# Optimization experiments

Measured on AMD Instinct MI355X. Metric: run time of the kernel, lower is better.

## Reference

```python
import jax, jax.numpy as jnp
import numpy as np

T = 2048        # tokens (single causal sequence)
HID = 2048      # hidden_size
H = 16          # num_heads
DN = 128        # qk_nope_head_dim
DR = 64         # qk_rope_head_dim
DQK = DN + DR   # 192
DV = 128        # v_head_dim
QLR = 1536      # q_lora_rank
KVLR = 512      # kv_lora_rank
INTER = 10944   # intermediate_size
EPS = 1e-6
THETA = 10000.0


def rmsnorm(x, w, eps=EPS):
    var = jnp.mean(jnp.square(x), axis=-1, keepdims=True)
    return x * jax.lax.rsqrt(var + eps) * w


def _deinterleave(x):
    # view(b,h,d//2,2).transpose(3,2).reshape(b,h,d): [x0,x2,...,x1,x3,...]
    t, h, d = x.shape
    return x.reshape(t, h, d // 2, 2).swapaxes(-1, -2).reshape(t, h, d)


def _rotate_half(x):
    d = x.shape[-1]
    return jnp.concatenate([-x[..., d // 2:], x[..., :d // 2]], axis=-1)


def setup_inputs() -> dict:
    key = jax.random.key(0)
    ks = jax.random.split(key, 12)
    s = 0.02
    hidden_states = jax.random.normal(ks[0], (T, HID), jnp.float32)
    # real rotary cos/sin tables over the rope slice
    inv_freq = 1.0 / (THETA ** (np.arange(0, DR, 2, dtype=np.float64) / DR))
    freqs = np.outer(np.arange(T, dtype=np.float64), inv_freq)
    emb = np.concatenate([freqs, freqs], axis=-1)  # (T, DR)
    cos = jnp.asarray(np.cos(emb), jnp.float32)[:, None, :]
    sin = jnp.asarray(np.sin(emb), jnp.float32)[:, None, :]
    return {
        "hidden_states": hidden_states,
        "cos": cos,
        "sin": sin,
        "ln_input": jnp.ones((HID,), jnp.float32),
        "w_q_a": jax.random.normal(ks[1], (QLR, HID), jnp.float32) * s,
        "ln_q_a": jnp.ones((QLR,), jnp.float32),
        "w_q_b": jax.random.normal(ks[2], (H * DQK, QLR), jnp.float32) * s,
        "w_kv_a": jax.random.normal(ks[3], (KVLR + DR, HID), jnp.float32) * s,
        "ln_kv_a": jnp.ones((KVLR,), jnp.float32),
        "w_kv_b": jax.random.normal(ks[4], (H * (DN + DV), KVLR), jnp.float32) * s,
        "w_o": jax.random.normal(ks[5], (HID, H * DV), jnp.float32) * s,
        "ln_post": jnp.ones((HID,), jnp.float32),
        "w_gate": jax.random.normal(ks[6], (INTER, HID), jnp.float32) * s,
        "w_up": jax.random.normal(ks[7], (INTER, HID), jnp.float32) * s,
        "w_down": jax.random.normal(ks[8], (HID, INTER), jnp.float32) * s,
    }


def reference(hidden_states, cos, sin, ln_input, w_q_a, ln_q_a, w_q_b,
              w_kv_a, ln_kv_a, w_kv_b, w_o, ln_post, w_gate, w_up, w_down):
    residual = hidden_states
    h = rmsnorm(hidden_states, ln_input)

    # --- MLA attention ---
    # low-rank Q: q_a -> rmsnorm -> q_b
    q = rmsnorm(h @ w_q_a.T, ln_q_a) @ w_q_b.T          # (T, H*DQK)
    q = q.reshape(T, H, DQK)
    q_nope, q_pe = q[..., :DN], q[..., DN:]

    # low-rank KV with shared rope part (MQA-style)
    ckv = h @ w_kv_a.T                                   # (T, KVLR+DR)
    c_kv, k_pe = ckv[:, :KVLR], ckv[:, KVLR:]
    c_kv = rmsnorm(c_kv, ln_kv_a)
    kv = (c_kv @ w_kv_b.T).reshape(T, H, DN + DV)
    k_nope, v = kv[..., :DN], kv[..., DN:]

    # interleaved RoPE on the rope slice
    qp = _deinterleave(q_pe)
    kp = _deinterleave(k_pe.reshape(T, 1, DR))
    q_emb = qp * cos + _rotate_half(qp) * sin            # (T,H,DR)
    k_emb = kp * cos + _rotate_half(kp) * sin            # (T,1,DR)

    q_full = jnp.concatenate([q_nope, q_emb], axis=-1)                          # (T,H,DQK)
    k_full = jnp.concatenate([k_nope, jnp.broadcast_to(k_emb, (T, H, DR))], -1)  # (T,H,DQK)

    scaling = DQK ** -0.5
    scores = jnp.einsum('qhd,khd->hqk', q_full, k_full) * scaling  # (H,T,T)
    idx = jnp.arange(T)
    causal = idx[None, :] <= idx[:, None]                          # (q,k)
    scores = jnp.where(causal[None, :, :], scores, jnp.finfo(scores.dtype).min)
    probs = jax.nn.softmax(scores, axis=-1)
    attn = jnp.einsum('hqk,khd->qhd', probs, v)                    # (T,H,DV)
    attn_out = attn.reshape(T, H * DV) @ w_o.T                     # (T,HID)

    residual = residual + attn_out
    h2 = rmsnorm(residual, ln_post)

    # --- gated MLP (SiLU) ---
    mlp = (jax.nn.silu(h2 @ w_gate.T) * (h2 @ w_up.T)) @ w_down.T
    return residual + mlp
```

## Files before the change

### kernel.cpp

```cpp
#include <hip/hip_runtime.h>
#include <hip/hip_bf16.h>
#include <cstdint>
#include <cstddef>

#define T_SEQ 2048
#define NH 16
#define DQK 192
#define DV 128

typedef __attribute__((ext_vector_type(8))) short short8;
typedef __attribute__((ext_vector_type(4))) float f32x4;

__device__ __forceinline__ void load_lds_16(const void* g, void* l) {
    __builtin_amdgcn_global_load_lds(
        (const __attribute__((address_space(1))) void*)g,
        (__attribute__((address_space(3))) void*)l, 16, 0, 0);
}

__global__ void cvt_pad(const float* __restrict__ in, __hip_bfloat16* __restrict__ out,
                        long n_real, long n_pad) {
    long i = ((long)blockIdx.x * blockDim.x + threadIdx.x) * 4;
    const long stride = (long)gridDim.x * blockDim.x * 4;
    for (; i < n_pad; i += stride) {
        float v0 = 0.f, v1 = 0.f, v2 = 0.f, v3 = 0.f;
        if (i < n_real) {
            const float4 v = *(const float4*)(in + i);
            v0 = v.x; v1 = v.y; v2 = v.z; v3 = v.w;
        }
        out[i + 0] = __float2bfloat16(v0);
        out[i + 1] = __float2bfloat16(v1);
        out[i + 2] = __float2bfloat16(v2);
        out[i + 3] = __float2bfloat16(v3);
    }
}

__global__ __launch_bounds__(256) void rmsnorm_bf16(
    const float* __restrict__ x, const float* __restrict__ w,
    __hip_bfloat16* __restrict__ y, int D, int ldx) {
    const int row = blockIdx.x;
    const float* xr = x + (size_t)row * ldx;
    float ss = 0.f;
    for (int i = threadIdx.x; i < D; i += 256) { float v = xr[i]; ss += v * v; }
    for (int off = 32; off > 0; off >>= 1) ss += __shfl_down(ss, off);
    __shared__ float part[4];
    if ((threadIdx.x & 63) == 0) part[threadIdx.x >> 6] = ss;
    __syncthreads();
    const float tot = part[0] + part[1] + part[2] + part[3];
    const float rs = rsqrtf(tot / (float)D + 1e-6f);
    __hip_bfloat16* yr = y + (size_t)row * D;
    for (int i = threadIdx.x; i < D; i += 256)
        yr[i] = __float2bfloat16(xr[i] * rs * w[i]);
}

template<int EPI>
__global__ __launch_bounds__(256) void gemm_bt(
    const __hip_bfloat16* __restrict__ A, const __hip_bfloat16* __restrict__ B,
    float* __restrict__ Cf, __hip_bfloat16* __restrict__ Cb,
    const float* __restrict__ Add, int N, int K) {
    __shared__ __hip_bfloat16 As[128 * 32];
    __shared__ __hip_bfloat16 Bs[128 * 32];
    const int tid = threadIdx.x;
    const int wave = tid >> 6;
    const int lane = tid & 63;
    const int col = lane & 15;
    const int quad = lane >> 4;
    const long bm = (long)blockIdx.y * 128;
    const long bn = (long)blockIdx.x * 128;
    const int wm = (wave & 1) * 64;
    const int wn = (wave >> 1) * 64;

    const int f0 = tid * 8;
    const int r0 = f0 >> 5, c0 = f0 & 31;
    const int f1 = (256 + tid) * 8;
    const int r1 = f1 >> 5, c1 = f1 & 31;
    __hip_bfloat16* dstA0 = &As[wave * 512];
    __hip_bfloat16* dstA1 = &As[2048 + wave * 512];
    __hip_bfloat16* dstB0 = &Bs[wave * 512];
    __hip_bfloat16* dstB1 = &Bs[2048 + wave * 512];

    f32x4 acc[4][4];
    for (int i = 0; i < 4; i++)
        for (int j = 0; j < 4; j++) acc[i][j] = (f32x4){0.f, 0.f, 0.f, 0.f};

    for (int k0 = 0; k0 < K; k0 += 32) {
        __syncthreads();
        load_lds_16(A + (bm + r0) * (long)K + k0 + c0, dstA0);
        load_lds_16(A + (bm + r1) * (long)K + k0 + c1, dstA1);
        load_lds_16(B + (bn + r0) * (long)K + k0 + c0, dstB0);
        load_lds_16(B + (bn + r1) * (long)K + k0 + c1, dstB1);
        __syncthreads();
        short8 a[4], b[4];
        for (int i = 0; i < 4; i++)
            a[i] = *(const short8*)&As[(wm + 16 * i + col) * 32 + quad * 8];
        for (int j = 0; j < 4; j++)
            b[j] = *(const short8*)&Bs[(wn + 16 * j + col) * 32 + quad * 8];
        for (int i = 0; i < 4; i++)
            for (int j = 0; j < 4; j++)
                acc[i][j] = __builtin_amdgcn_mfma_f32_16x16x32_bf16(a[i], b[j], acc[i][j], 0, 0, 0);
    }

    for (int i = 0; i < 4; i++) {
        const long gm = bm + wm + 16 * i + quad * 4;
        for (int j = 0; j < 4; j++) {
            const long gn = bn + wn + 16 * j + col;
            if (gn < N) {
                for (int r = 0; r < 4; r++) {
                    const long idx = (gm + r) * (long)N + gn;
                    const float a0 = acc[i][j][r];
                    if (EPI == 0) {
                        Cf[idx] = a0;
                    } else if (EPI == 1) {
                        Cf[idx] = a0 + Add[idx];
                    } else if (EPI == 2) {
                        const float s = a0 / (1.f + __expf(-a0));
                        Cb[idx] = __float2bfloat16(s);
                    } else {
                        const float g = __bfloat162float(Cb[idx]);
                        Cb[idx] = __float2bfloat16(g * a0);
                    }
                }
            }
        }
    }
}

__global__ __launch_bounds__(256) void rope_pack(
    const float* __restrict__ q, const float* __restrict__ ckv,
    const float* __restrict__ kv,
    const float* __restrict__ cosT, const float* __restrict__ sinT,
    __hip_bfloat16* __restrict__ qf, __hip_bfloat16* __restrict__ kf,
    __hip_bfloat16* __restrict__ vt) {
    const int t = blockIdx.x;
    const int tid = threadIdx.x;
    __shared__ float kemb[64];
    if (tid < 64) {
        const int j = tid;
        const int m = j & 31;
        const float c = cosT[t * 64 + j], s = sinT[t * 64 + j];
        const float x0 = ckv[(size_t)t * 576 + 512 + 2 * m];
        const float x1 = ckv[(size_t)t * 576 + 512 + 2 * m + 1];
        kemb[j] = (j >= 32) ? (x1 * c + x0 * s) : (x0 * c - x1 * s);
    }
    __syncthreads();
    for (int h = 0; h < NH; h++) {
        const size_t qrow = ((size_t)h * T_SEQ + t) * DQK;
        if (tid < 128) {
            qf[qrow + tid] = __float2bfloat16(q[(size_t)t * 3072 + h * DQK + tid]);
            kf[qrow + tid] = __float2bfloat16(kv[(size_t)t * 4096 + h * 256 + tid]);
            vt[((size_t)h * 128 + tid) * T_SEQ + t] =
                __float2bfloat16(kv[(size_t)t * 4096 + h * 256 + 128 + tid]);
        } else if (tid < 192) {
            const int j = tid - 128;
            const int m = j & 31;
            const float c = cosT[t * 64 + j], s = sinT[t * 64 + j];
            const float x0 = q[(size_t)t * 3072 + h * DQK + 128 + 2 * m];
            const float x1 = q[(size_t)t * 3072 + h * DQK + 128 + 2 * m + 1];
            const float v = (j >= 32) ? (x1 * c + x0 * s) : (x0 * c - x1 * s);
            qf[qrow + 128 + j] = __float2bfloat16(v);
            kf[qrow + 128 + j] = __float2bfloat16(kemb[j]);
        }
    }
}

#define KROW 208
#define VROW 80
#define PROW 72

__global__ __launch_bounds__(256) void flash_attn(
    const __hip_bfloat16* __restrict__ Qf, const __hip_bfloat16* __restrict__ Kf,
    const __hip_bfloat16* __restrict__ Vt, __hip_bfloat16* __restrict__ Oout) {
    const int h = blockIdx.y;
    const int qt = (h < 8) ? blockIdx.x : (31 - blockIdx.x);
    const int tid = threadIdx.x;
    const int wave = tid >> 6;
    const int lane = tid & 63;
    const int col = lane & 15;
    const int quad = lane >> 4;
    const int q0b = qt * 64;
    const int q0w = q0b + wave * 16;

    __shared__ __hip_bfloat16 Ks[1792 * 8];
    __shared__ __hip_bfloat16 Vs[128 * VROW];
    __shared__ __hip_bfloat16 Plds[4][16 * PROW];

    const __hip_bfloat16* Qh = Qf + (size_t)h * T_SEQ * DQK;
    const __hip_bfloat16* Kh = Kf + (size_t)h * T_SEQ * DQK;
    const __hip_bfloat16* Vh = Vt + (size_t)h * DV * T_SEQ;

    short8 qfr[6];
    for (int d = 0; d < 6; d++)
        qfr[d] = *(const short8*)&Qh[(size_t)(q0w + col) * DQK + d * 32 + quad * 8];

    float m_i[4], l_i[4];
    f32x4 o[8];
    for (int r = 0; r < 4; r++) { m_i[r] = -INFINITY; l_i[r] = 0.f; }
    for (int dt = 0; dt < 8; dt++) o[dt] = (f32x4){0.f, 0.f, 0.f, 0.f};

    const float scaling = 0.07216878364870323f;
    const int kc_end = q0b + 64;

    for (int kc = 0; kc < kc_end; kc += 64) {
        __syncthreads();
        #pragma unroll
        for (int it = 0; it < 7; it++) {
            const int L = (it * 256 + tid) * 16;
            const int row = L / 416;
            const int c16 = (L % 416) / 16;
            const __hip_bfloat16* src = (row < 64 && c16 < 24)
                ? Kh + (size_t)(kc + row) * DQK + c16 * 8 : Kh;
            load_lds_16(src, (char*)Ks + it * 4096 + wave * 1024);
        }
        #pragma unroll
        for (int it = 0; it < 5; it++) {
            const int L = (it * 256 + tid) * 16;
            const int row = L / 160;
            const int c16 = (L % 160) / 16;
            const __hip_bfloat16* src = (c16 < 8)
                ? Vh + (size_t)row * T_SEQ + kc + c16 * 8 : Vh;
            load_lds_16(src, (char*)Vs + it * 4096 + wave * 1024);
        }
        __syncthreads();

        f32x4 s[4];
        for (int f = 0; f < 4; f++) s[f] = (f32x4){0.f, 0.f, 0.f, 0.f};
        for (int d = 0; d < 6; d++)
            for (int f = 0; f < 4; f++) {
                short8 b = *(const short8*)&Ks[(f * 16 + col) * KROW + d * 32 + quad * 8];
                s[f] = __builtin_amdgcn_mfma_f32_16x16x32_bf16(qfr[d], b, s[f], 0, 0, 0);
            }

        float mx[4];
        for (int r = 0; r < 4; r++) mx[r] = -1e30f;
        for (int f = 0; f < 4; f++)
            for (int r = 0; r < 4; r++) {
                const int rowq = q0w + quad * 4 + r;
                const int kcol = kc + f * 16 + col;
                float v = s[f][r] * scaling;
                if (kcol > rowq) v = -1e30f;
                s[f][r] = v;
                mx[r] = fmaxf(mx[r], v);
            }
        for (int off = 1; off < 16; off <<= 1)
            for (int r = 0; r < 4; r++)
                mx[r] = fmaxf(mx[r], __shfl_xor(mx[r], off));
        float alpha[4], rsum[4];
        for (int r = 0; r < 4; r++) {
            const float mnew = fmaxf(m_i[r], mx[r]);
            alpha[r] = __expf(m_i[r] - mnew);
            m_i[r] = mnew;
            rsum[r] = 0.f;
        }
        float p[4][4];
        for (int f = 0; f < 4; f++)
            for (int r = 0; r < 4; r++) {
                p[f][r] = __expf(s[f][r] - m_i[r]);
                rsum[r] += p[f][r];
            }
        for (int off = 1; off < 16; off <<= 1)
            for (int r = 0; r < 4; r++)
                rsum[r] += __shfl_xor(rsum[r], off);
        for (int r = 0; r < 4; r++) l_i[r] = l_i[r] * alpha[r] + rsum[r];
        for (int dt = 0; dt < 8; dt++)
            for (int r = 0; r < 4; r++) o[dt][r] *= alpha[r];

        for (int f = 0; f < 4; f++)
            for (int r = 0; r < 4; r++)
                Plds[wave][(quad * 4 + r) * PROW + f * 16 + col] = __float2bfloat16(p[f][r]);
        asm volatile("s_waitcnt lgkmcnt(0)" ::: "memory");
        short8 pa[2];
        for (int c = 0; c < 2; c++)
            pa[c] = *(const short8*)&Plds[wave][col * PROW + c * 32 + quad * 8];

        for (int dt = 0; dt < 8; dt++)
            for (int c = 0; c < 2; c++) {
                short8 bv = *(const short8*)&Vs[(dt * 16 + col) * VROW + c * 32 + quad * 8];
                o[dt] = __builtin_amdgcn_mfma_f32_16x16x32_bf16(pa[c], bv, o[dt], 0, 0, 0);
            }
    }

    for (int r = 0; r < 4; r++) {
        const int row = q0w + quad * 4 + r;
        const float inv = 1.f / l_i[r];
        for (int dt = 0; dt < 8; dt++)
            Oout[(size_t)row * (NH * DV) + h * DV + dt * 16 + col] =
                __float2bfloat16(o[dt][r] * inv);
    }
}

__global__ void fill_f32(float* __restrict__ y, long n, float v) {
    long i = (long)blockIdx.x * blockDim.x + threadIdx.x;
    const long st = (long)gridDim.x * blockDim.x;
    for (; i < n; i += st) y[i] = v;
}

extern "C" void kernel_launch(void* const* d_in, const int* in_sizes, int n_in,
                              void* d_out, int out_size, void* d_ws, size_t ws_size,
                              hipStream_t stream) {
    const float* hidden   = (const float*)d_in[0];
    const float* cosT     = (const float*)d_in[1];
    const float* sinT     = (const float*)d_in[2];
    const float* ln_input = (const float*)d_in[3];
    const float* w_q_a    = (const float*)d_in[4];
    const float* ln_q_a   = (const float*)d_in[5];
    const float* w_q_b    = (const float*)d_in[6];
    const float* w_kv_a   = (const float*)d_in[7];
    const float* ln_kv_a  = (const float*)d_in[8];
    const float* w_kv_b   = (const float*)d_in[9];
    const float* w_o      = (const float*)d_in[10];
    const float* ln_post  = (const float*)d_in[11];
    const float* w_gate   = (const float*)d_in[12];
    const float* w_up     = (const float*)d_in[13];
    const float* w_down   = (const float*)d_in[14];
    float* out = (float*)d_out;

    char* ws = (char*)d_ws;
    size_t off = 0;
    auto alloc = [&](size_t bytes) -> char* {
        off = (off + 255) & ~(size_t)255;
        char* p = ws + off;
        off += bytes;
        return p;
    };

    char* W_ = alloc(11008l * 2048 * 2);
    char* A_ = alloc(2048l * 3072 * 4);
    char* B_ = alloc(2048l * 10944 * 2);
    char* C_ = alloc(2048l * 576 * 4);
    char* D_ = alloc(2048l * 2048 * 4);
    char* E_ = alloc((16l * 2048 * 192 + 16l * 128 * 2048) * 2);

    if (off > ws_size) {
        fill_f32<<<2048, 256, 0, stream>>>(out, (long)out_size, -77777.0f);
        return;
    }

    auto* Wb     = (__hip_bfloat16*)W_;
    auto* h_b    = (__hip_bfloat16*)A_;
    auto* q_f    = (float*)A_;
    auto* attn_b = (__hip_bfloat16*)A_;
    auto* h2_b   = (__hip_bfloat16*)A_;
    auto* qa_f   = (float*)B_;
    auto* kv_f   = (float*)B_;
    auto* gate_b = (__hip_bfloat16*)B_;
    auto* ckv_f  = (float*)C_;
    auto* qan_b  = (__hip_bfloat16*)D_;
    auto* ckvn_b = (__hip_bfloat16*)(D_ + 2048l * 1536 * 2);
    auto* kf_b   = (__hip_bfloat16*)D_;
    auto* res_f  = (float*)D_;
    auto* qf_b   = (__hip_bfloat16*)E_;
    auto* vt_b   = (__hip_bfloat16*)(E_ + 16l * 2048 * 192 * 2);

    auto cvt = [&](const float* src, long n_real, long n_pad) {
        cvt_pad<<<2048, 256, 0, stream>>>(src, Wb, n_real, n_pad);
    };
    auto gemm = [&](int EPI, const __hip_bfloat16* A, float* Cf, __hip_bfloat16* Cb,
                    const float* Add, int N, int Npad, int K) {
        dim3 g(Npad / 128, 16);
        if (EPI == 0)      gemm_bt<0><<<g, 256, 0, stream>>>(A, Wb, Cf, Cb, Add, N, K);
        else if (EPI == 1) gemm_bt<1><<<g, 256, 0, stream>>>(A, Wb, Cf, Cb, Add, N, K);
        else if (EPI == 2) gemm_bt<2><<<g, 256, 0, stream>>>(A, Wb, Cf, Cb, Add, N, K);
        else               gemm_bt<3><<<g, 256, 0, stream>>>(A, Wb, Cf, Cb, Add, N, K);
    };

    rmsnorm_bf16<<<2048, 256, 0, stream>>>(hidden, ln_input, h_b, 2048, 2048);
    cvt(w_q_a, 1536l * 2048, 1536l * 2048);
    gemm(0, h_b, qa_f, nullptr, nullptr, 1536, 1536, 2048);
    cvt(w_kv_a, 576l * 2048, 640l * 2048);
    gemm(0, h_b, ckv_f, nullptr, nullptr, 576, 640, 2048);
    rmsnorm_bf16<<<2048, 256, 0, stream>>>(qa_f, ln_q_a, qan_b, 1536, 1536);
    rmsnorm_bf16<<<2048, 256, 0, stream>>>(ckv_f, ln_kv_a, ckvn_b, 512, 576);
    cvt(w_q_b, 3072l * 1536, 3072l * 1536);
    gemm(0, qan_b, q_f, nullptr, nullptr, 3072, 3072, 1536);
    cvt(w_kv_b, 4096l * 512, 4096l * 512);
    gemm(0, ckvn_b, kv_f, nullptr, nullptr, 4096, 4096, 512);
    rope_pack<<<2048, 256, 0, stream>>>(q_f, ckv_f, kv_f, cosT, sinT, qf_b, kf_b, vt_b);
    flash_attn<<<dim3(32, 16), 256, 0, stream>>>(qf_b, kf_b, vt_b, attn_b);
    cvt(w_o, 2048l * 2048, 2048l * 2048);
    gemm(1, attn_b, res_f, nullptr, hidden, 2048, 2048, 2048);

    rmsnorm_bf16<<<2048, 256, 0, stream>>>(res_f, ln_post, h2_b, 2048, 2048);
    cvt(w_gate, 10944l * 2048, 11008l * 2048);
    gemm(2, h2_b, nullptr, gate_b, nullptr, 10944, 11008, 2048);
    cvt(w_up, 10944l * 2048, 11008l * 2048);
    gemm(3, h2_b, nullptr, gate_b, nullptr, 10944, 11008, 2048);
    cvt(w_down, 2048l * 10944, 2048l * 10944);
    gemm(1, gate_b, out, nullptr, res_f, 2048, 2048, 10944);
}
```

Measured before the change: 1.222 ms.

## Add split-K with atomic accumulation for the narrow projection GEMMs

The GEMM kernel gains a grid z dimension that splits the K loop, plus a new epilogue that accumulates partial tiles into an fp32 output with atomicAdd. The q/kv projections, the output projection and the down projection now use 2–8 K-splits, with outputs either zero-filled or pre-seeded with the residual via a device copy. The aim is to fill the GPU's compute units on GEMMs whose 128x128 tile grid is small, especially the long-K down projection. In exchange it adds fill/copy passes, atomic traffic and a non-deterministic summation order.

```diff
diff --git a/kernel.cpp b/kernel.cpp
--- a/kernel.cpp
+++ b/kernel.cpp
@@ -68,6 +68,9 @@
     const long bn = (long)blockIdx.x * 128;
     const int wm = (wave & 1) * 64;
     const int wn = (wave >> 1) * 64;
+    const int ksub = K / gridDim.z;
+    const int kbeg = blockIdx.z * ksub;
+    const int kend = kbeg + ksub;
 
     const int f0 = tid * 8;
     const int r0 = f0 >> 5, c0 = f0 & 31;
@@ -82,7 +85,7 @@
     for (int i = 0; i < 4; i++)
         for (int j = 0; j < 4; j++) acc[i][j] = (f32x4){0.f, 0.f, 0.f, 0.f};
 
-    for (int k0 = 0; k0 < K; k0 += 32) {
+    for (int k0 = kbeg; k0 < kend; k0 += 32) {
         __syncthreads();
         load_lds_16(A + (bm + r0) * (long)K + k0 + c0, dstA0);
         load_lds_16(A + (bm + r1) * (long)K + k0 + c1, dstA1);
@@ -114,9 +117,11 @@
                     } else if (EPI == 2) {
                         const float s = a0 / (1.f + __expf(-a0));
                         Cb[idx] = __float2bfloat16(s);
-                    } else {
+                    } else if (EPI == 3) {
                         const float g = __bfloat162float(Cb[idx]);
                         Cb[idx] = __float2bfloat16(g * a0);
+                    } else {
+                        atomicAdd(&Cf[idx], a0);
                     }
                 }
             }
@@ -354,35 +359,45 @@
         cvt_pad<<<2048, 256, 0, stream>>>(src, Wb, n_real, n_pad);
     };
     auto gemm = [&](int EPI, const __hip_bfloat16* A, float* Cf, __hip_bfloat16* Cb,
-                    const float* Add, int N, int Npad, int K) {
-        dim3 g(Npad / 128, 16);
+                    const float* Add, int N, int Npad, int K, int splits) {
+        dim3 g(Npad / 128, 16, splits);
         if (EPI == 0)      gemm_bt<0><<<g, 256, 0, stream>>>(A, Wb, Cf, Cb, Add, N, K);
         else if (EPI == 1) gemm_bt<1><<<g, 256, 0, stream>>>(A, Wb, Cf, Cb, Add, N, K);
         else if (EPI == 2) gemm_bt<2><<<g, 256, 0, stream>>>(A, Wb, Cf, Cb, Add, N, K);
-        else               gemm_bt<3><<<g, 256, 0, stream>>>(A, Wb, Cf, Cb, Add, N, K);
+        else if (EPI == 3) gemm_bt<3><<<g, 256, 0, stream>>>(A, Wb, Cf, Cb, Add, N, K);
+        else               gemm_bt<4><<<g, 256, 0, stream>>>(A, Wb, Cf, Cb, Add, N, K);
+    };
+    auto zero = [&](float* p, long n) {
+        fill_f32<<<2048, 256, 0, stream>>>(p, n, 0.f);
     };
 
     rmsnorm_bf16<<<2048, 256, 0, stream>>>(hidden, ln_input, h_b, 2048, 2048);
     cvt(w_q_a, 1536l * 2048, 1536l * 2048);
-    gemm(0, h_b, qa_f, nullptr, nullptr, 1536, 1536, 2048);
+    zero(qa_f, 2048l * 1536);
+    gemm(4, h_b, qa_f, nullptr, nullptr, 1536, 1536, 2048, 4);
     cvt(w_kv_a, 576l * 2048, 640l * 2048);
-    gemm(0, h_b, ckv_f, nullptr, nullptr, 576, 640, 2048);
+    zero(ckv_f, 2048l * 576);
+    gemm(4, h_b, ckv_f, nullptr, nullptr, 576, 640, 2048, 8);
     rmsnorm_bf16<<<2048, 256, 0, stream>>>(qa_f, ln_q_a, qan_b, 1536, 1536);
     rmsnorm_bf16<<<2048, 256, 0, stream>>>(ckv_f, ln_kv_a, ckvn_b, 512, 576);
     cvt(w_q_b, 3072l * 1536, 3072l * 1536);
-    gemm(0, qan_b, q_f, nullptr, nullptr, 3072, 3072, 1536);
+    zero(q_f, 2048l * 3072);
+    gemm(4, qan_b, q_f, nullptr, nullptr, 3072, 3072, 1536, 2);
     cvt(w_kv_b, 4096l * 512, 4096l * 512);
-    gemm(0, ckvn_b, kv_f, nullptr, nullptr, 4096, 4096, 512);
+    zero(kv_f, 2048l * 4096);
+    gemm(4, ckvn_b, kv_f, nullptr, nullptr, 4096, 4096, 512, 2);
     rope_pack<<<2048, 256, 0, stream>>>(q_f, ckv_f, kv_f, cosT, sinT, qf_b, kf_b, vt_b);
     flash_attn<<<dim3(32, 16), 256, 0, stream>>>(qf_b, kf_b, vt_b, attn_b);
     cvt(w_o, 2048l * 2048, 2048l * 2048);
-    gemm(1, attn_b, res_f, nullptr, hidden, 2048, 2048, 2048);
+    hipMemcpyAsync(res_f, hidden, 2048l * 2048 * 4, hipMemcpyDeviceToDevice, stream);
+    gemm(4, attn_b, res_f, nullptr, nullptr, 2048, 2048, 2048, 4);
 
     rmsnorm_bf16<<<2048, 256, 0, stream>>>(res_f, ln_post, h2_b, 2048, 2048);
     cvt(w_gate, 10944l * 2048, 11008l * 2048);
-    gemm(2, h2_b, nullptr, gate_b, nullptr, 10944, 11008, 2048);
+    gemm(2, h2_b, nullptr, gate_b, nullptr, 10944, 11008, 2048, 1);
     cvt(w_up, 10944l * 2048, 11008l * 2048);
-    gemm(3, h2_b, nullptr, gate_b, nullptr, 10944, 11008, 2048);
+    gemm(3, h2_b, nullptr, gate_b, nullptr, 10944, 11008, 2048, 1);
     cvt(w_down, 2048l * 10944, 2048l * 10944);
-    gemm(1, gate_b, out, nullptr, res_f, 2048, 2048, 10944);
-}
+    hipMemcpyAsync(out, res_f, 2048l * 2048 * 4, hipMemcpyDeviceToDevice, stream);
+    gemm(4, gate_b, out, nullptr, nullptr, 2048, 2048, 10944, 6);
+}
```

Result: slower. 1.258 ms (+3.0%).

## Split-K small GEMMs with reduction kernels and fuse gate/up into one GEMM

Applied to the files above, without the earlier changes.

Adds a grid.z split-K mode to the bf16 GEMM for the kv_a, o_proj and down projections. Partial results go to float buffers, and a separate reduce_parts kernel sums them and adds the residual. This raises the block count on GEMMs whose 2D grids underfill the GPU, at the cost of extra partial-buffer traffic and extra launches. Gate and up weights are interleaved in 16-row groups by a new conversion kernel, so one GEMM computes both and applies SiLU(gate)*up in its epilogue. That removes the separate up-GEMM pass that read back and rewrote the bf16 gate buffer.

```diff
diff --git a/kernel.cpp b/kernel.cpp
--- a/kernel.cpp
+++ b/kernel.cpp
@@ -32,6 +32,28 @@
         out[i + 2] = __float2bfloat16(v2);
         out[i + 3] = __float2bfloat16(v3);
     }
+}
+
+__global__ __launch_bounds__(256) void cvt_gu(
+    const float* __restrict__ g, const float* __restrict__ u,
+    __hip_bfloat16* __restrict__ out, int row_off) {
+    const int R = blockIdx.x;
+    const int group = R >> 5, pos = R & 31;
+    const int ll = group * 16 + (pos & 15);
+    const bool valid = ll < 5472;
+    const float* src = (pos < 16) ? g : u;
+    const float* srow = src + (size_t)(row_off + ll) * 2048;
+    __hip_bfloat16* orow = out + (size_t)R * 2048;
+    const int i0 = threadIdx.x * 8;
+    float4 a = {0, 0, 0, 0}, b = {0, 0, 0, 0};
+    if (valid) {
+        a = *(const float4*)(srow + i0);
+        b = *(const float4*)(srow + i0 + 4);
+    }
+    orow[i0 + 0] = __float2bfloat16(a.x); orow[i0 + 1] = __float2bfloat16(a.y);
+    orow[i0 + 2] = __float2bfloat16(a.z); orow[i0 + 3] = __float2bfloat16(a.w);
+    orow[i0 + 4] = __float2bfloat16(b.x); orow[i0 + 5] = __float2bfloat16(b.y);
+    orow[i0 + 6] = __float2bfloat16(b.z); orow[i0 + 7] = __float2bfloat16(b.w);
 }
 
 __global__ __launch_bounds__(256) void rmsnorm_bf16(
@@ -52,11 +74,26 @@
         yr[i] = __float2bfloat16(xr[i] * rs * w[i]);
 }
 
+__global__ void reduce_parts(const float* __restrict__ parts, long pstride, int np,
+                             const float* __restrict__ base, float* __restrict__ dst,
+                             long n) {
+    long i = ((long)blockIdx.x * blockDim.x + threadIdx.x) * 4;
+    const long st = (long)gridDim.x * blockDim.x * 4;
+    for (; i < n; i += st) {
+        float4 acc = base ? *(const float4*)(base + i) : (float4){0, 0, 0, 0};
+        for (int z = 0; z < np; z++) {
+            const float4 p = *(const float4*)(parts + z * pstride + i);
+            acc.x += p.x; acc.y += p.y; acc.z += p.z; acc.w += p.w;
+        }
+        *(float4*)(dst + i) = acc;
+    }
+}
+
 template<int EPI>
 __global__ __launch_bounds__(256) void gemm_bt(
     const __hip_bfloat16* __restrict__ A, const __hip_bfloat16* __restrict__ B,
     float* __restrict__ Cf, __hip_bfloat16* __restrict__ Cb,
-    const float* __restrict__ Add, int N, int K) {
+    int N, int K, int ldc, long pstride) {
     __shared__ __hip_bfloat16 As[128 * 32];
     __shared__ __hip_bfloat16 Bs[128 * 32];
     const int tid = threadIdx.x;
@@ -68,6 +105,9 @@
     const long bn = (long)blockIdx.x * 128;
     const int wm = (wave & 1) * 64;
     const int wn = (wave >> 1) * 64;
+    const int ksub = K / gridDim.z;
+    const int kbeg = blockIdx.z * ksub;
+    const int kend = kbeg + ksub;
 
     const int f0 = tid * 8;
     const int r0 = f0 >> 5, c0 = f0 & 31;
@@ -82,7 +122,7 @@
     for (int i = 0; i < 4; i++)
         for (int j = 0; j < 4; j++) acc[i][j] = (f32x4){0.f, 0.f, 0.f, 0.f};
 
-    for (int k0 = 0; k0 < K; k0 += 32) {
+    for (int k0 = kbeg; k0 < kend; k0 += 32) {
         __syncthreads();
         load_lds_16(A + (bm + r0) * (long)K + k0 + c0, dstA0);
         load_lds_16(A + (bm + r1) * (long)K + k0 + c1, dstA1);
@@ -99,24 +139,28 @@
                 acc[i][j] = __builtin_amdgcn_mfma_f32_16x16x32_bf16(a[i], b[j], acc[i][j], 0, 0, 0);
     }
 
-    for (int i = 0; i < 4; i++) {
-        const long gm = bm + wm + 16 * i + quad * 4;
-        for (int j = 0; j < 4; j++) {
-            const long gn = bn + wn + 16 * j + col;
-            if (gn < N) {
-                for (int r = 0; r < 4; r++) {
-                    const long idx = (gm + r) * (long)N + gn;
-                    const float a0 = acc[i][j][r];
-                    if (EPI == 0) {
-                        Cf[idx] = a0;
-                    } else if (EPI == 1) {
-                        Cf[idx] = a0 + Add[idx];
-                    } else if (EPI == 2) {
-                        const float s = a0 / (1.f + __expf(-a0));
-                        Cb[idx] = __float2bfloat16(s);
-                    } else {
-                        const float g = __bfloat162float(Cb[idx]);
-                        Cb[idx] = __float2bfloat16(g * a0);
+    if (EPI == 0) {
+        float* Cz = Cf + (long)blockIdx.z * pstride;
+        for (int i = 0; i < 4; i++) {
+            const long gm = bm + wm + 16 * i + quad * 4;
+            for (int j = 0; j < 4; j++) {
+                const long gn = bn + wn + 16 * j + col;
+                if (gn < N)
+                    for (int r = 0; r < 4; r++)
+                        Cz[(gm + r) * (long)ldc + gn] = acc[i][j][r];
+            }
+        }
+    } else {
+        for (int i = 0; i < 4; i++) {
+            const long gm = bm + wm + 16 * i + quad * 4;
+            for (int jp = 0; jp < 2; jp++) {
+                const long gn = (((bn + wn) >> 5) + jp) * 16 + col;
+                if (gn < N) {
+                    for (int r = 0; r < 4; r++) {
+                        const float g = acc[i][2 * jp][r];
+                        const float u = acc[i][2 * jp + 1][r];
+                        const float s = g / (1.f + __expf(-g));
+                        Cb[(gm + r) * (long)ldc + gn] = __float2bfloat16(s * u);
                     }
                 }
             }
@@ -323,7 +367,7 @@
     };
 
     char* W_ = alloc(11008l * 2048 * 2);
-    char* A_ = alloc(2048l * 3072 * 4);
+    char* A_ = alloc(2048l * 2048 * 4 * 2);
     char* B_ = alloc(2048l * 10944 * 2);
     char* C_ = alloc(2048l * 576 * 4);
     char* D_ = alloc(2048l * 2048 * 4);
@@ -334,55 +378,63 @@
         return;
     }
 
-    auto* Wb     = (__hip_bfloat16*)W_;
-    auto* h_b    = (__hip_bfloat16*)A_;
-    auto* q_f    = (float*)A_;
-    auto* attn_b = (__hip_bfloat16*)A_;
-    auto* h2_b   = (__hip_bfloat16*)A_;
-    auto* qa_f   = (float*)B_;
-    auto* kv_f   = (float*)B_;
-    auto* gate_b = (__hip_bfloat16*)B_;
-    auto* ckv_f  = (float*)C_;
-    auto* qan_b  = (__hip_bfloat16*)D_;
-    auto* ckvn_b = (__hip_bfloat16*)(D_ + 2048l * 1536 * 2);
-    auto* kf_b   = (__hip_bfloat16*)D_;
-    auto* res_f  = (float*)D_;
-    auto* qf_b   = (__hip_bfloat16*)E_;
-    auto* vt_b   = (__hip_bfloat16*)(E_ + 16l * 2048 * 192 * 2);
+    auto* Wb       = (__hip_bfloat16*)W_;
+    auto* h_b      = (__hip_bfloat16*)A_;
+    auto* q_f      = (float*)A_;
+    auto* attn_b   = (__hip_bfloat16*)A_;
+    auto* h2_b     = (__hip_bfloat16*)A_;
+    auto* dn_parts = (float*)A_;
+    auto* qa_f     = (float*)B_;
+    auto* kva_parts= (float*)(B_ + (1l << 24));
+    auto* kv_f     = (float*)B_;
+    auto* o_parts  = (float*)B_;
+    auto* act_b    = (__hip_bfloat16*)B_;
+    auto* ckv_f    = (float*)C_;
+    auto* qan_b    = (__hip_bfloat16*)D_;
+    auto* ckvn_b   = (__hip_bfloat16*)(D_ + 2048l * 1536 * 2);
+    auto* kf_b     = (__hip_bfloat16*)D_;
+    auto* res_f    = (float*)D_;
+    auto* qf_b     = (__hip_bfloat16*)E_;
+    auto* vt_b     = (__hip_bfloat16*)(E_ + 16l * 2048 * 192 * 2);
 
     auto cvt = [&](const float* src, long n_real, long n_pad) {
         cvt_pad<<<2048, 256, 0, stream>>>(src, Wb, n_real, n_pad);
     };
-    auto gemm = [&](int EPI, const __hip_bfloat16* A, float* Cf, __hip_bfloat16* Cb,
-                    const float* Add, int N, int Npad, int K) {
-        dim3 g(Npad / 128, 16);
-        if (EPI == 0)      gemm_bt<0><<<g, 256, 0, stream>>>(A, Wb, Cf, Cb, Add, N, K);
-        else if (EPI == 1) gemm_bt<1><<<g, 256, 0, stream>>>(A, Wb, Cf, Cb, Add, N, K);
-        else if (EPI == 2) gemm_bt<2><<<g, 256, 0, stream>>>(A, Wb, Cf, Cb, Add, N, K);
-        else               gemm_bt<3><<<g, 256, 0, stream>>>(A, Wb, Cf, Cb, Add, N, K);
+    auto gemm0 = [&](const __hip_bfloat16* A, float* Cf, int N, int Npad, int K,
+                     int splits, long pstride) {
+        dim3 g(Npad / 128, 16, splits);
+        gemm_bt<0><<<g, 256, 0, stream>>>(A, Wb, Cf, nullptr, N, K, N, pstride);
     };
 
     rmsnorm_bf16<<<2048, 256, 0, stream>>>(hidden, ln_input, h_b, 2048, 2048);
     cvt(w_q_a, 1536l * 2048, 1536l * 2048);
-    gemm(0, h_b, qa_f, nullptr, nullptr, 1536, 1536, 2048);
+    gemm0(h_b, qa_f, 1536, 1536, 2048, 1, 0);
     cvt(w_kv_a, 576l * 2048, 640l * 2048);
-    gemm(0, h_b, ckv_f, nullptr, nullptr, 576, 640, 2048);
+    gemm0(h_b, kva_parts, 576, 640, 2048, 4, 2048l * 576);
+    reduce_parts<<<2048, 256, 0, stream>>>(kva_parts, 2048l * 576, 4, nullptr,
+                                           ckv_f, 2048l * 576);
     rmsnorm_bf16<<<2048, 256, 0, stream>>>(qa_f, ln_q_a, qan_b, 1536, 1536);
     rmsnorm_bf16<<<2048, 256, 0, stream>>>(ckv_f, ln_kv_a, ckvn_b, 512, 576);
     cvt(w_q_b, 3072l * 1536, 3072l * 1536);
-    gemm(0, qan_b, q_f, nullptr, nullptr, 3072, 3072, 1536);
+    gemm0(qan_b, q_f, 3072, 3072, 1536, 1, 0);
     cvt(w_kv_b, 4096l * 512, 4096l * 512);
-    gemm(0, ckvn_b, kv_f, nullptr, nullptr, 4096, 4096, 512);
+    gemm0(ckvn_b, kv_f, 4096, 4096, 512, 1, 0);
     rope_pack<<<2048, 256, 0, stream>>>(q_f, ckv_f, kv_f, cosT, sinT, qf_b, kf_b, vt_b);
     flash_attn<<<dim3(32, 16), 256, 0, stream>>>(qf_b, kf_b, vt_b, attn_b);
     cvt(w_o, 2048l * 2048, 2048l * 2048);
-    gemm(1, attn_b, res_f, nullptr, hidden, 2048, 2048, 2048);
+    gemm0(attn_b, o_parts, 2048, 2048, 2048, 2, 2048l * 2048);
+    reduce_parts<<<2048, 256, 0, stream>>>(o_parts, 2048l * 2048, 2, hidden,
+                                           res_f, 2048l * 2048);
 
     rmsnorm_bf16<<<2048, 256, 0, stream>>>(res_f, ln_post, h2_b, 2048, 2048);
-    cvt(w_gate, 10944l * 2048, 11008l * 2048);
-    gemm(2, h2_b, nullptr, gate_b, nullptr, 10944, 11008, 2048);
-    cvt(w_up, 10944l * 2048, 11008l * 2048);
-    gemm(3, h2_b, nullptr, gate_b, nullptr, 10944, 11008, 2048);
+    for (int half = 0; half < 2; half++) {
+        cvt_gu<<<11008, 256, 0, stream>>>(w_gate, w_up, Wb, half * 5472);
+        dim3 g(86, 16, 1);
+        gemm_bt<5><<<g, 256, 0, stream>>>(h2_b, Wb, nullptr,
+                                          act_b + half * 5472, 5472, 2048, 10944, 0);
+    }
     cvt(w_down, 2048l * 10944, 2048l * 10944);
-    gemm(1, gate_b, out, nullptr, res_f, 2048, 2048, 10944);
-}
+    gemm0(act_b, dn_parts, 2048, 2048, 10944, 2, 2048l * 2048);
+    reduce_parts<<<2048, 256, 0, stream>>>(dn_parts, 2048l * 2048, 2, res_f,
+                                           out, 2048l * 2048);
+}
```

Result: faster. 1.075 ms (-12.0%).
